# Kernel optimization log

Hardware: AMD Instinct MI355X
Metric: run time of the kernel (lower is better)

## Reference

```python
import jax, jax.numpy as jnp
import numpy as np
import math

D_MODEL = 1024
N_HEAD = 16


def setup_inputs() -> dict:
    key = jax.random.key(0)
    ks = jax.random.split(key, 5)
    x = jax.random.normal(ks[0], (2, 2048, D_MODEL), dtype=jnp.float32)
    # Linear params (torch Linear: y = x @ W.T + b); store as [in, out] for einsum
    s1 = 1.0 / math.sqrt(D_MODEL)
    W_qkv = jax.random.uniform(ks[1], (D_MODEL, 3 * D_MODEL), jnp.float32, -s1, s1)
    b_qkv = jax.random.uniform(ks[2], (3 * D_MODEL,), jnp.float32, -s1, s1)
    W_out = jax.random.uniform(ks[3], (D_MODEL, D_MODEL), jnp.float32, -s1, s1)
    b_out = jax.random.uniform(ks[4], (D_MODEL,), jnp.float32, -s1, s1)
    return {"x": x, "W_qkv": W_qkv, "b_qkv": b_qkv, "W_out": W_out, "b_out": b_out}


def reference(x, W_qkv, b_qkv, W_out, b_out):
    B, L, D = x.shape
    H = N_HEAD
    hd = D // H
    qkv = x @ W_qkv + b_qkv                      # [B, L, 3D]
    q, k, v = jnp.split(qkv, 3, axis=-1)
    # [B, H, L, hd]
    q = q.reshape(B, L, H, hd).transpose(0, 2, 1, 3)
    k = k.reshape(B, L, H, hd).transpose(0, 2, 1, 3)
    v = v.reshape(B, L, H, hd).transpose(0, 2, 1, 3)
    scale = 1.0 / math.sqrt(hd)
    scores = jnp.einsum('bhqd,bhkd->bhqk', q, k) * scale   # [B, H, L, L]
    causal = jnp.tril(jnp.ones((L, L), dtype=bool))
    scores = jnp.where(causal, scores, jnp.float32(-jnp.inf))
    probs = jax.nn.softmax(scores, axis=-1)
    out = jnp.einsum('bhqk,bhkd->bhqd', probs, v)          # [B, H, L, hd]
    out = out.transpose(0, 2, 1, 3).reshape(B, L, D)
    out = out @ W_out + b_out
    return jnp.squeeze(out)
```

## Files before the change

kernel.cpp:

```cpp
#include <hip/hip_runtime.h>
#include <hip/hip_bf16.h>

#define SEQ    2048
#define NHEAD  16
#define HD     64
#define DMODEL 1024

using bf16 = __hip_bfloat16;
using short8 = __attribute__((ext_vector_type(8))) short;
using short4v = __attribute__((ext_vector_type(4))) short;
using f32x4  = __attribute__((ext_vector_type(4))) float;

__device__ __forceinline__ float fast_exp2(float x) {
  return __builtin_amdgcn_exp2f(x);
}
#define WAIT_LGKM0() __builtin_amdgcn_s_waitcnt(0xC07F)

__device__ __forceinline__ void gload_lds16(const bf16* g, bf16* l) {
  __builtin_amdgcn_global_load_lds(
      (const __attribute__((address_space(1))) void*)g,
      (__attribute__((address_space(3))) void*)l, 16, 0, 0);
}


__global__ void prep_k(const float* __restrict__ x, bf16* __restrict__ xb,
                       const float* __restrict__ Wqkv, bf16* __restrict__ WqkvT,
                       const float* __restrict__ Wout, bf16* __restrict__ WoutT) {
  __shared__ bf16 tile[32][33];
  const int id = blockIdx.x, tid = threadIdx.x;
  if (id < 2048) {
    int i = (id * 256 + tid) * 8;
    bf16 tmp[8];
    #pragma unroll
    for (int j = 0; j < 8; ++j) tmp[j] = __float2bfloat16(x[i + j]);
    *(short8*)&xb[i] = *(short8*)tmp;
    return;
  }
  const float* in; bf16* out; int R, C, tx32, ty32;
  if (id < 2048 + 3072) {
    int t = id - 2048; in = Wqkv; out = WqkvT; R = 1024; C = 3072;
    tx32 = t % 96; ty32 = t / 96;
  } else {
    int t = id - 5120; in = Wout; out = WoutT; R = 1024; C = 1024;
    tx32 = t % 32; ty32 = t / 32;
  }
  int c0 = tx32 * 32, r0 = ty32 * 32;
  int tx = tid & 31, ty = tid >> 5;
  #pragma unroll
  for (int i = ty; i < 32; i += 8)
    tile[i][tx] = __float2bfloat16(in[(size_t)(r0 + i) * C + c0 + tx]);
  __syncthreads();
  #pragma unroll
  for (int i = ty; i < 32; i += 8)
    out[(size_t)(c0 + i) * R + r0 + tx] = tile[tx][i];
}

template <int MODE>
__global__ __launch_bounds__(256)
void gemm_bt(const bf16* __restrict__ A, const bf16* __restrict__ BT,
             const float* __restrict__ bias,
             bf16* __restrict__ out0, bf16* __restrict__ out1,
             bf16* __restrict__ out2, float* __restrict__ outf) {
  constexpr int K = 1024;
  __shared__ __align__(16) bf16 As[128 * 32];
  __shared__ __align__(16) bf16 Bs[128 * 32];
  const int tid = threadIdx.x;
  const int wave = tid >> 6, lane = tid & 63;
  const int quad = lane >> 4, l16 = lane & 15;
  const int waveM = (wave >> 1) * 64, waveN = (wave & 1) * 64;
  const int m0 = blockIdx.x * 128, n0 = blockIdx.y * 128;
  const bool swapped = (MODE == 0) && (n0 < 2048);
  const int srow = (lane >> 2);
  const int scol = (((lane & 3) ^ ((lane >> 3) & 3)) * 8);
  const int q8   = (quad ^ ((l16 >> 1) & 3)) * 8;

  const f32x4 zero4 = {0.f, 0.f, 0.f, 0.f};
  f32x4 acc[4][4];
  #pragma unroll
  for (int i = 0; i < 4; ++i)
    #pragma unroll
    for (int j = 0; j < 4; ++j) acc[i][j] = zero4;

  for (int k0 = 0; k0 < K; k0 += 32) {
    __syncthreads();
    #pragma unroll
    for (int half = 0; half < 2; ++half) {
      int grow = half * 64 + wave * 16 + srow;
      gload_lds16(&A [(size_t)(m0 + grow) * K + k0 + scol],
                  &As[(half * 64 + wave * 16) * 32]);
      gload_lds16(&BT[(size_t)(n0 + grow) * K + k0 + scol],
                  &Bs[(half * 64 + wave * 16) * 32]);
    }
    __syncthreads();
    short8 af[4], bfm[4];
    #pragma unroll
    for (int mt = 0; mt < 4; ++mt)
      af[mt] = *(const short8*)&As[(waveM + mt * 16 + l16) * 32 + q8];
    #pragma unroll
    for (int nt = 0; nt < 4; ++nt)
      bfm[nt] = *(const short8*)&Bs[(waveN + nt * 16 + l16) * 32 + q8];
    if (swapped) {
      #pragma unroll
      for (int mt = 0; mt < 4; ++mt)
        #pragma unroll
        for (int nt = 0; nt < 4; ++nt)
          acc[mt][nt] = __builtin_amdgcn_mfma_f32_16x16x32_bf16(
              bfm[nt], af[mt], acc[mt][nt], 0, 0, 0);
    } else {
      #pragma unroll
      for (int mt = 0; mt < 4; ++mt)
        #pragma unroll
        for (int nt = 0; nt < 4; ++nt)
          acc[mt][nt] = __builtin_amdgcn_mfma_f32_16x16x32_bf16(
              af[mt], bfm[nt], acc[mt][nt], 0, 0, 0);
    }
  }

  if (MODE == 1) {
    #pragma unroll
    for (int nt = 0; nt < 4; ++nt) {
      int n = n0 + waveN + nt * 16 + l16;
      float bvv = bias[n];
      #pragma unroll
      for (int mt = 0; mt < 4; ++mt) {
        #pragma unroll
        for (int r = 0; r < 4; ++r) {
          int m = m0 + waveM + mt * 16 + quad * 4 + r;
          outf[(size_t)m * 1024 + n] = acc[mt][nt][r] + bvv;
        }
      }
    }
  } else if (swapped) {
    #pragma unroll
    for (int nt = 0; nt < 4; ++nt) {
      int nb = n0 + waveN + nt * 16 + quad * 4;
      const f32x4 b4 = *(const f32x4*)&bias[nb];
      int oo = nb & 1023;
      int h = oo >> 6, cc = oo & 63;
      bf16* outp = (nb >> 10) ? out1 : out0;
      #pragma unroll
      for (int mt = 0; mt < 4; ++mt) {
        int m = m0 + waveM + mt * 16 + l16;
        int bb = m >> 11, l = m & 2047;
        bf16 tmp[4];
        #pragma unroll
        for (int r = 0; r < 4; ++r)
          tmp[r] = __float2bfloat16(acc[mt][nt][r] + b4[r]);
        *(short4v*)&outp[((size_t)(bb * NHEAD + h) * SEQ + l) * HD + cc] =
            *(short4v*)tmp;
      }
    }
  } else {
    #pragma unroll
    for (int nt = 0; nt < 4; ++nt) {
      int n = n0 + waveN + nt * 16 + l16;
      float bvv = bias[n];
      int oo = n & 1023;
      int h = oo >> 6, cc = oo & 63;
      #pragma unroll
      for (int mt = 0; mt < 4; ++mt) {
        int m = m0 + waveM + mt * 16 + quad * 4;
        int bb = m >> 11, l = m & 2047;
        bf16 tmp[4];
        #pragma unroll
        for (int r = 0; r < 4; ++r)
          tmp[r] = __float2bfloat16(acc[mt][nt][r] + bvv);
        *(short4v*)&out2[((size_t)(bb * NHEAD + h) * HD + cc) * SEQ + l] =
            *(short4v*)tmp;
      }
    }
  }
}

__global__ __launch_bounds__(256, 3)
void attn_k(const bf16* __restrict__ Q, const bf16* __restrict__ Kb,
            const bf16* __restrict__ VT, bf16* __restrict__ O) {
  __shared__ __align__(16) bf16 Ks[2][2][64 * 32];
  __shared__ __align__(16) bf16 Vs[2][2][64 * 32];
  __shared__ __align__(16) bf16 Plds[4][16][72];
  const int tid = threadIdx.x;
  const int wave = tid >> 6, lane = tid & 63;
  const int quad = lane >> 4, l16 = lane & 15;
  const int srow = lane >> 2;
  const int scol = (((lane & 3) ^ ((lane >> 3) & 3)) * 8);
  const int q8   = (quad ^ ((l16 >> 1) & 3)) * 8;
  const int id = blockIdx.x;
  const int bh = id & 31;
  const int qt = 31 - (id >> 5);
  const int b = bh >> 4, h = bh & 15;

  const bf16* Qp = Q  + (size_t)bh * SEQ * HD;
  const bf16* Kp = Kb + (size_t)bh * SEQ * HD;
  const bf16* Vp = VT + (size_t)bh * HD * SEQ;

  const f32x4 zero4 = {0.f, 0.f, 0.f, 0.f};
  const float c = 0.18033688011112042f;
  const float mc = 8.0f * c;

  const int q0w = qt * 64 + wave * 16;
  const int q_lane = q0w + l16;
  const int ntiles = qt + 1;

  short8 qf0 = *(const short8*)&Qp[(size_t)(q0w + l16) * HD + quad * 8];
  short8 qf1 = *(const short8*)&Qp[(size_t)(q0w + l16) * HD + 32 + quad * 8];

  f32x4 oacc[4];
  #pragma unroll
  for (int dt = 0; dt < 4; ++dt) oacc[dt] = zero4;
  float l4[4] = {0.f, 0.f, 0.f, 0.f};

  {
    const int k0 = 0;
    #pragma unroll
    for (int hh = 0; hh < 2; ++hh)
      gload_lds16(&Kp[(size_t)(k0 + wave * 16 + srow) * HD + hh * 32 + scol],
                  &Ks[0][hh][(wave * 16) * 32]);
    #pragma unroll
    for (int ch = 0; ch < 2; ++ch)
      gload_lds16(&Vp[(size_t)(wave * 16 + srow) * SEQ + k0 + ch * 32 + scol],
                  &Vs[0][ch][(wave * 16) * 32]);
  }
  __syncthreads();

  for (int t = 0; t < ntiles; ++t) {
    const int buf = t & 1;
    if (t + 1 < ntiles) {
      const int k1 = (t + 1) << 6, nb = buf ^ 1;
      #pragma unroll
      for (int hh = 0; hh < 2; ++hh)
        gload_lds16(&Kp[(size_t)(k1 + wave * 16 + srow) * HD + hh * 32 + scol],
                    &Ks[nb][hh][(wave * 16) * 32]);
      #pragma unroll
      for (int ch = 0; ch < 2; ++ch)
        gload_lds16(&Vp[(size_t)(wave * 16 + srow) * SEQ + k1 + ch * 32 + scol],
                    &Vs[nb][ch][(wave * 16) * 32]);
    }
    const int k0 = t << 6;

    f32x4 s[4];
    __builtin_amdgcn_s_setprio(1);
    #pragma unroll
    for (int g = 0; g < 4; ++g) {
      short8 ka = *(const short8*)&Ks[buf][0][(g * 16 + l16) * 32 + q8];
      short8 kb = *(const short8*)&Ks[buf][1][(g * 16 + l16) * 32 + q8];
      f32x4 sg = zero4;
      sg = __builtin_amdgcn_mfma_f32_16x16x32_bf16(ka, qf0, sg, 0, 0, 0);
      sg = __builtin_amdgcn_mfma_f32_16x16x32_bf16(kb, qf1, sg, 0, 0, 0);
      s[g] = sg;
    }
    __builtin_amdgcn_s_setprio(0);

    if (t == ntiles - 1) {
      #pragma unroll
      for (int g = 0; g < 4; ++g)
        #pragma unroll
        for (int r = 0; r < 4; ++r) {
          int k = k0 + g * 16 + quad * 4 + r;
          s[g][r] = (k <= q_lane) ? s[g][r] : -__builtin_inff();
        }
    }

    #pragma unroll
    for (int g = 0; g < 4; ++g) {
      bf16 pb[4];
      #pragma unroll
      for (int r = 0; r < 4; ++r) {
        float p = fast_exp2(__builtin_fmaf(s[g][r], c, -mc));
        l4[r] += p;
        pb[r] = __float2bfloat16(p);
      }
      *(short4v*)&Plds[wave][l16][g * 16 + quad * 4] = *(short4v*)pb;
    }
    WAIT_LGKM0();

    __builtin_amdgcn_s_setprio(1);
    #pragma unroll
    for (int ch = 0; ch < 2; ++ch) {
      short8 pf = *(const short8*)&Plds[wave][l16][ch * 32 + quad * 8];
      #pragma unroll
      for (int dt = 0; dt < 4; ++dt) {
        short8 vf = *(const short8*)&Vs[buf][ch][(dt * 16 + l16) * 32 + q8];
        oacc[dt] = __builtin_amdgcn_mfma_f32_16x16x32_bf16(vf, pf, oacc[dt], 0, 0, 0);
      }
    }
    __builtin_amdgcn_s_setprio(0);
    __syncthreads();
  }

  float l_i = (l4[0] + l4[1]) + (l4[2] + l4[3]);
  l_i += __shfl_xor(l_i, 16, 64);
  l_i += __shfl_xor(l_i, 32, 64);
  float inv = 1.f / l_i;

  #pragma unroll
  for (int dt = 0; dt < 4; ++dt) {
    bf16 ob[4];
    #pragma unroll
    for (int r = 0; r < 4; ++r) ob[r] = __float2bfloat16(oacc[dt][r] * inv);
    *(short4v*)&Plds[wave][l16][dt * 16 + quad * 4] = *(short4v*)ob;
  }
  WAIT_LGKM0();
  {
    int row = lane >> 2;
    int col = (lane & 3) * 16;
    short8 o0 = *(const short8*)&Plds[wave][row][col];
    short8 o1 = *(const short8*)&Plds[wave][row][col + 8];
    size_t base = ((size_t)(b * SEQ + q0w + row)) * DMODEL + h * HD + col;
    *(short8*)&O[base]     = o0;
    *(short8*)&O[base + 8] = o1;
  }
}

extern "C" void kernel_launch(void* const* d_in, const int* in_sizes, int n_in,
                              void* d_out, int out_size, void* d_ws, size_t ws_size,
                              hipStream_t stream) {
  const float* x    = (const float*)d_in[0];
  const float* Wqkv = (const float*)d_in[1];
  const float* bqkv = (const float*)d_in[2];
  const float* Wout = (const float*)d_in[3];
  const float* bout = (const float*)d_in[4];
  float* out = (float*)d_out;

  char* ws = (char*)d_ws;
  const size_t MB = 1024 * 1024;
  char* big    = ws + 16384;
  bf16* Kbuf   = (bf16*)(big);
  bf16* VTb    = (bf16*)(big + 8 * MB);
  bf16* xb     = (bf16*)(big + 16 * MB);
  bf16* AO     = (bf16*)(big + 16 * MB);
  bf16* WqkvT  = (bf16*)(big + 24 * MB);
  bf16* WoutT  = (bf16*)(big + 30 * MB);
  bf16* Qb     = (bf16*)d_out;

  prep_k<<<6144, 256, 0, stream>>>(x, xb, Wqkv, WqkvT, Wout, WoutT);
  gemm_bt<0><<<dim3(4096 / 128, 3072 / 128), 256, 0, stream>>>(
      xb, WqkvT, bqkv, Qb, Kbuf, VTb, nullptr);
  attn_k<<<1024, 256, 0, stream>>>(Qb, Kbuf, VTb, AO);
  gemm_bt<1><<<dim3(4096 / 128, 1024 / 128), 256, 0, stream>>>(
      AO, WoutT, bout, nullptr, nullptr, nullptr, out);
}
```

Baseline: 184.4 us.

## Replace QKV GEMM with 256x256-tile, 4-stage pipelined, XCD-aware kernel

Adds a dedicated QKV projection kernel that uses 512 threads and 256x256 output tiles. It streams K-slices through a 4-deep LDS ring buffer using global_load_lds and counted waitcnt, and raises wave priority around the MFMA block. Blocks are mapped so that each XCD gets a contiguous M/N region, which improves L2 reuse. The aim is to cut global traffic per FLOP and hide load latency. In exchange it uses much more LDS and registers, and its 192 blocks leave some imbalance across CUs. The output GEMM is split out into its own non-templated kernel.

```diff
diff --git a/kernel.cpp b/kernel.cpp
--- a/kernel.cpp
+++ b/kernel.cpp
@@ -55,12 +55,140 @@
     out[(size_t)(c0 + i) * R + r0 + tx] = tile[tx][i];
 }
 
-template <int MODE>
+__global__ __launch_bounds__(512, 2)
+void gemm_qkv256(const bf16* __restrict__ A, const bf16* __restrict__ BT,
+                 const float* __restrict__ bias,
+                 bf16* __restrict__ outQ, bf16* __restrict__ outK,
+                 bf16* __restrict__ outV) {
+  constexpr int K = 1024;
+  __shared__ __align__(16) bf16 SA[4][8192];
+  __shared__ __align__(16) bf16 SB[4][8192];
+  const int tid = threadIdx.x;
+  const int wave = tid >> 6, lane = tid & 63;
+  const int quad = lane >> 4, l16 = lane & 15;
+  const int srow = lane >> 2;
+  const int scol = (((lane & 3) ^ ((lane >> 3) & 3)) * 8);
+  const int q8   = (quad ^ ((l16 >> 1) & 3)) * 8;
+  const int waveM = (wave >> 2) * 128, waveN = (wave & 3) * 64;
+
+  const int L = blockIdx.x;
+  const int xcd = L & 7, idx = L >> 3;
+  const int m0 = ((xcd >> 2) * 8 + (idx & 7)) * 256;
+  const int n0 = ((xcd & 3) * 3 + (idx >> 3)) * 256;
+  const bool swapped = n0 < 2048;
+
+  const bf16* aS = A  + (size_t)(m0 + wave * 16 + srow) * K + scol;
+  const bf16* bS = BT + (size_t)(n0 + wave * 16 + srow) * K + scol;
+  bf16* dA = &SA[0][(wave * 16) * 32];
+  bf16* dB = &SB[0][(wave * 16) * 32];
+
+#define STAGE_SLICE(sp)                                                     \
+  {                                                                         \
+    const int rg_ = (sp) & 3, kk_ = (sp) * 32;                              \
+    gload_lds16(aS + kk_,                dA + rg_ * 8192);                  \
+    gload_lds16(aS + 128 * K + kk_,      dA + rg_ * 8192 + 128 * 32);       \
+    gload_lds16(bS + kk_,                dB + rg_ * 8192);                  \
+    gload_lds16(bS + 128 * K + kk_,      dB + rg_ * 8192 + 128 * 32);       \
+  }
+
+  const f32x4 zero4 = {0.f, 0.f, 0.f, 0.f};
+  f32x4 acc[8][4];
+  #pragma unroll
+  for (int i = 0; i < 8; ++i)
+    #pragma unroll
+    for (int j = 0; j < 4; ++j) acc[i][j] = zero4;
+
+  STAGE_SLICE(0);
+  STAGE_SLICE(1);
+  STAGE_SLICE(2);
+
+#define PHASE(s_, WAITN_, DOSTAGE_)                                         \
+  {                                                                         \
+    if (DOSTAGE_) STAGE_SLICE((s_) + 3);                                    \
+    asm volatile("" ::: "memory");                                          \
+    __builtin_amdgcn_s_waitcnt(0xF70 | (WAITN_));   \
+    __builtin_amdgcn_s_barrier();                                           \
+    asm volatile("" ::: "memory");                                          \
+    const bf16* pa = &SA[(s_) & 3][(waveM + l16) * 32 + q8];                \
+    const bf16* pb = &SB[(s_) & 3][(waveN + l16) * 32 + q8];                \
+    short8 af[8], bfr[4];                                                   \
+    _Pragma("unroll")                                                       \
+    for (int mt = 0; mt < 8; ++mt) af[mt] = *(const short8*)(pa + mt * 512);\
+    _Pragma("unroll")                                                       \
+    for (int nt = 0; nt < 4; ++nt) bfr[nt] = *(const short8*)(pb + nt * 512);\
+    __builtin_amdgcn_s_setprio(1);                                          \
+    if (swapped) {                                                          \
+      _Pragma("unroll")                                                     \
+      for (int mt = 0; mt < 8; ++mt)                                        \
+        _Pragma("unroll")                                                   \
+        for (int nt = 0; nt < 4; ++nt)                                      \
+          acc[mt][nt] = __builtin_amdgcn_mfma_f32_16x16x32_bf16(            \
+              bfr[nt], af[mt], acc[mt][nt], 0, 0, 0);                       \
+    } else {                                                                \
+      _Pragma("unroll")                                                     \
+      for (int mt = 0; mt < 8; ++mt)                                        \
+        _Pragma("unroll")                                                   \
+        for (int nt = 0; nt < 4; ++nt)                                      \
+          acc[mt][nt] = __builtin_amdgcn_mfma_f32_16x16x32_bf16(            \
+              af[mt], bfr[nt], acc[mt][nt], 0, 0, 0);                       \
+    }                                                                       \
+    __builtin_amdgcn_s_setprio(0);                                          \
+    asm volatile("" ::: "memory");                                          \
+    __builtin_amdgcn_s_barrier();                                           \
+    asm volatile("" ::: "memory");                                          \
+  }
+
+  #pragma unroll 1
+  for (int s = 0; s < 29; ++s) PHASE(s, 12, true);
+  PHASE(29, 8, false);
+  PHASE(30, 4, false);
+  PHASE(31, 0, false);
+#undef PHASE
+#undef STAGE_SLICE
+
+  if (swapped) {
+    bf16* outp = (n0 >= 1024) ? outK : outQ;
+    #pragma unroll
+    for (int nt = 0; nt < 4; ++nt) {
+      const int nb = n0 + waveN + nt * 16 + quad * 4;
+      const f32x4 b4 = *(const f32x4*)&bias[nb];
+      const int oo = nb & 1023, h = oo >> 6, cc = oo & 63;
+      #pragma unroll
+      for (int mt = 0; mt < 8; ++mt) {
+        const int m = m0 + waveM + mt * 16 + l16;
+        const int bb = m >> 11, l = m & 2047;
+        bf16 tmp[4];
+        #pragma unroll
+        for (int r = 0; r < 4; ++r)
+          tmp[r] = __float2bfloat16(acc[mt][nt][r] + b4[r]);
+        *(short4v*)&outp[((size_t)(bb * NHEAD + h) * SEQ + l) * HD + cc] =
+            *(short4v*)tmp;
+      }
+    }
+  } else {
+    #pragma unroll
+    for (int nt = 0; nt < 4; ++nt) {
+      const int n = n0 + waveN + nt * 16 + l16;
+      const float bv = bias[n];
+      const int oo = n & 1023, h = oo >> 6, cc = oo & 63;
+      #pragma unroll
+      for (int mt = 0; mt < 8; ++mt) {
+        const int m = m0 + waveM + mt * 16 + quad * 4;
+        const int bb = m >> 11, l = m & 2047;
+        bf16 tmp[4];
+        #pragma unroll
+        for (int r = 0; r < 4; ++r)
+          tmp[r] = __float2bfloat16(acc[mt][nt][r] + bv);
+        *(short4v*)&outV[((size_t)(bb * NHEAD + h) * HD + cc) * SEQ + l] =
+            *(short4v*)tmp;
+      }
+    }
+  }
+}
+
 __global__ __launch_bounds__(256)
-void gemm_bt(const bf16* __restrict__ A, const bf16* __restrict__ BT,
-             const float* __restrict__ bias,
-             bf16* __restrict__ out0, bf16* __restrict__ out1,
-             bf16* __restrict__ out2, float* __restrict__ outf) {
+void gemm_out128(const bf16* __restrict__ A, const bf16* __restrict__ BT,
+                 const float* __restrict__ bias, float* __restrict__ outf) {
   constexpr int K = 1024;
   __shared__ __align__(16) bf16 As[128 * 32];
   __shared__ __align__(16) bf16 Bs[128 * 32];
@@ -69,7 +197,6 @@
   const int quad = lane >> 4, l16 = lane & 15;
   const int waveM = (wave >> 1) * 64, waveN = (wave & 1) * 64;
   const int m0 = blockIdx.x * 128, n0 = blockIdx.y * 128;
-  const bool swapped = (MODE == 0) && (n0 < 2048);
   const int srow = (lane >> 2);
   const int scol = (((lane & 3) ^ ((lane >> 3) & 3)) * 8);
   const int q8   = (quad ^ ((l16 >> 1) & 3)) * 8;
@@ -99,74 +226,24 @@
     #pragma unroll
     for (int nt = 0; nt < 4; ++nt)
       bfm[nt] = *(const short8*)&Bs[(waveN + nt * 16 + l16) * 32 + q8];
-    if (swapped) {
-      #pragma unroll
-      for (int mt = 0; mt < 4; ++mt)
-        #pragma unroll
-        for (int nt = 0; nt < 4; ++nt)
-          acc[mt][nt] = __builtin_amdgcn_mfma_f32_16x16x32_bf16(
-              bfm[nt], af[mt], acc[mt][nt], 0, 0, 0);
-    } else {
-      #pragma unroll
-      for (int mt = 0; mt < 4; ++mt)
-        #pragma unroll
-        for (int nt = 0; nt < 4; ++nt)
-          acc[mt][nt] = __builtin_amdgcn_mfma_f32_16x16x32_bf16(
-              af[mt], bfm[nt], acc[mt][nt], 0, 0, 0);
-    }
-  }
-
-  if (MODE == 1) {
-    #pragma unroll
-    for (int nt = 0; nt < 4; ++nt) {
-      int n = n0 + waveN + nt * 16 + l16;
-      float bvv = bias[n];
-      #pragma unroll
-      for (int mt = 0; mt < 4; ++mt) {
-        #pragma unroll
-        for (int r = 0; r < 4; ++r) {
-          int m = m0 + waveM + mt * 16 + quad * 4 + r;
-          outf[(size_t)m * 1024 + n] = acc[mt][nt][r] + bvv;
-        }
-      }
-    }
-  } else if (swapped) {
-    #pragma unroll
-    for (int nt = 0; nt < 4; ++nt) {
-      int nb = n0 + waveN + nt * 16 + quad * 4;
-      const f32x4 b4 = *(const f32x4*)&bias[nb];
-      int oo = nb & 1023;
-      int h = oo >> 6, cc = oo & 63;
-      bf16* outp = (nb >> 10) ? out1 : out0;
-      #pragma unroll
-      for (int mt = 0; mt < 4; ++mt) {
-        int m = m0 + waveM + mt * 16 + l16;
-        int bb = m >> 11, l = m & 2047;
-        bf16 tmp[4];
-        #pragma unroll
-        for (int r = 0; r < 4; ++r)
-          tmp[r] = __float2bfloat16(acc[mt][nt][r] + b4[r]);
-        *(short4v*)&outp[((size_t)(bb * NHEAD + h) * SEQ + l) * HD + cc] =
-            *(short4v*)tmp;
-      }
-    }
-  } else {
-    #pragma unroll
-    for (int nt = 0; nt < 4; ++nt) {
-      int n = n0 + waveN + nt * 16 + l16;
-      float bvv = bias[n];
-      int oo = n & 1023;
-      int h = oo >> 6, cc = oo & 63;
-      #pragma unroll
-      for (int mt = 0; mt < 4; ++mt) {
-        int m = m0 + waveM + mt * 16 + quad * 4;
-        int bb = m >> 11, l = m & 2047;
-        bf16 tmp[4];
-        #pragma unroll
-        for (int r = 0; r < 4; ++r)
-          tmp[r] = __float2bfloat16(acc[mt][nt][r] + bvv);
-        *(short4v*)&out2[((size_t)(bb * NHEAD + h) * HD + cc) * SEQ + l] =
-            *(short4v*)tmp;
+    #pragma unroll
+    for (int mt = 0; mt < 4; ++mt)
+      #pragma unroll
+      for (int nt = 0; nt < 4; ++nt)
+        acc[mt][nt] = __builtin_amdgcn_mfma_f32_16x16x32_bf16(
+            af[mt], bfm[nt], acc[mt][nt], 0, 0, 0);
+  }
+
+  #pragma unroll
+  for (int nt = 0; nt < 4; ++nt) {
+    int n = n0 + waveN + nt * 16 + l16;
+    float bvv = bias[n];
+    #pragma unroll
+    for (int mt = 0; mt < 4; ++mt) {
+      #pragma unroll
+      for (int r = 0; r < 4; ++r) {
+        int m = m0 + waveM + mt * 16 + quad * 4 + r;
+        outf[(size_t)m * 1024 + n] = acc[mt][nt][r] + bvv;
       }
     }
   }
@@ -333,9 +410,8 @@
   bf16* Qb     = (bf16*)d_out;
 
   prep_k<<<6144, 256, 0, stream>>>(x, xb, Wqkv, WqkvT, Wout, WoutT);
-  gemm_bt<0><<<dim3(4096 / 128, 3072 / 128), 256, 0, stream>>>(
-      xb, WqkvT, bqkv, Qb, Kbuf, VTb, nullptr);
+  gemm_qkv256<<<192, 512, 0, stream>>>(xb, WqkvT, bqkv, Qb, Kbuf, VTb);
   attn_k<<<1024, 256, 0, stream>>>(Qb, Kbuf, VTb, AO);
-  gemm_bt<1><<<dim3(4096 / 128, 1024 / 128), 256, 0, stream>>>(
-      AO, WoutT, bout, nullptr, nullptr, nullptr, out);
-}
+  gemm_out128<<<dim3(4096 / 128, 1024 / 128), 256, 0, stream>>>(
+      AO, WoutT, bout, out);
+}
```

Result: slower. 371.2 us (+101.3%).

## Triple-buffer GEMM LDS loads and split QKV projection into two launches

Applied to the files above, without the earlier changes.

Replaces the single-buffered GEMM loop, which synchronized twice per k-step, with a three-stage LDS ring. Loads for step s+2 are issued before computing step s, using explicit vmcnt waits, raw barriers, and raised priority around the MFMAs. The QKV GEMM is split into a Q/K launch and a separate V^T launch, so each kernel has a uniform output layout instead of a per-block branch. The launch bound requests 3 blocks per CU, and LDS use triples, which may limit occupancy. An extra extra launch is added, and a stray dead load expression is left in the epilogue.

```diff
diff --git a/kernel.cpp b/kernel.cpp
--- a/kernel.cpp
+++ b/kernel.cpp
@@ -56,23 +56,38 @@
 }
 
 template <int MODE>
-__global__ __launch_bounds__(256)
-void gemm_bt(const bf16* __restrict__ A, const bf16* __restrict__ BT,
-             const float* __restrict__ bias,
-             bf16* __restrict__ out0, bf16* __restrict__ out1,
-             bf16* __restrict__ out2, float* __restrict__ outf) {
+__global__ __launch_bounds__(256, 3)
+void gemm_p(const bf16* __restrict__ A, const bf16* __restrict__ BT,
+            const float* __restrict__ bias,
+            bf16* __restrict__ o0, bf16* __restrict__ o1,
+            float* __restrict__ outf) {
   constexpr int K = 1024;
-  __shared__ __align__(16) bf16 As[128 * 32];
-  __shared__ __align__(16) bf16 Bs[128 * 32];
+  constexpr int NS = K / 32;
+  __shared__ __align__(16) bf16 SA[3][4096];
+  __shared__ __align__(16) bf16 SB[3][4096];
   const int tid = threadIdx.x;
   const int wave = tid >> 6, lane = tid & 63;
   const int quad = lane >> 4, l16 = lane & 15;
-  const int waveM = (wave >> 1) * 64, waveN = (wave & 1) * 64;
-  const int m0 = blockIdx.x * 128, n0 = blockIdx.y * 128;
-  const bool swapped = (MODE == 0) && (n0 < 2048);
-  const int srow = (lane >> 2);
+  const int srow = lane >> 2;
   const int scol = (((lane & 3) ^ ((lane >> 3) & 3)) * 8);
   const int q8   = (quad ^ ((l16 >> 1) & 3)) * 8;
+  const int waveM = (wave >> 1) * 64, waveN = (wave & 1) * 64;
+  const int m0 = blockIdx.x * 128;
+  const int n0 = (MODE == 2 ? 2048 : 0) + blockIdx.y * 128;
+
+  const bf16* aS = A  + (size_t)(m0 + wave * 16 + srow) * K + scol;
+  const bf16* bS = BT + (size_t)(n0 + wave * 16 + srow) * K + scol;
+  bf16* dA = &SA[0][(wave * 16) * 32];
+  bf16* dB = &SB[0][(wave * 16) * 32];
+
+#define STAGE(sp_, rg_)                                                    \
+  {                                                                        \
+    const int kk_ = (sp_) * 32;                                            \
+    gload_lds16(aS + kk_,           dA + (rg_) * 4096);                    \
+    gload_lds16(aS + 64 * K + kk_,  dA + (rg_) * 4096 + 64 * 32);          \
+    gload_lds16(bS + kk_,           dB + (rg_) * 4096);                    \
+    gload_lds16(bS + 64 * K + kk_,  dB + (rg_) * 4096 + 64 * 32);          \
+  }
 
   const f32x4 zero4 = {0.f, 0.f, 0.f, 0.f};
   f32x4 acc[4][4];
@@ -81,40 +96,53 @@
     #pragma unroll
     for (int j = 0; j < 4; ++j) acc[i][j] = zero4;
 
-  for (int k0 = 0; k0 < K; k0 += 32) {
-    __syncthreads();
-    #pragma unroll
-    for (int half = 0; half < 2; ++half) {
-      int grow = half * 64 + wave * 16 + srow;
-      gload_lds16(&A [(size_t)(m0 + grow) * K + k0 + scol],
-                  &As[(half * 64 + wave * 16) * 32]);
-      gload_lds16(&BT[(size_t)(n0 + grow) * K + k0 + scol],
-                  &Bs[(half * 64 + wave * 16) * 32]);
-    }
-    __syncthreads();
-    short8 af[4], bfm[4];
-    #pragma unroll
-    for (int mt = 0; mt < 4; ++mt)
-      af[mt] = *(const short8*)&As[(waveM + mt * 16 + l16) * 32 + q8];
-    #pragma unroll
-    for (int nt = 0; nt < 4; ++nt)
-      bfm[nt] = *(const short8*)&Bs[(waveN + nt * 16 + l16) * 32 + q8];
-    if (swapped) {
-      #pragma unroll
-      for (int mt = 0; mt < 4; ++mt)
-        #pragma unroll
-        for (int nt = 0; nt < 4; ++nt)
-          acc[mt][nt] = __builtin_amdgcn_mfma_f32_16x16x32_bf16(
-              bfm[nt], af[mt], acc[mt][nt], 0, 0, 0);
-    } else {
-      #pragma unroll
-      for (int mt = 0; mt < 4; ++mt)
-        #pragma unroll
-        for (int nt = 0; nt < 4; ++nt)
-          acc[mt][nt] = __builtin_amdgcn_mfma_f32_16x16x32_bf16(
-              af[mt], bfm[nt], acc[mt][nt], 0, 0, 0);
-    }
-  }
+  STAGE(0, 0);
+  STAGE(1, 1);
+
+#define PHASE(s_, rg_, WAITN_, DOSTAGE_, srg_)                             \
+  {                                                                        \
+    if (DOSTAGE_) STAGE((s_) + 2, (srg_));                                 \
+    asm volatile("" ::: "memory");                                         \
+    __builtin_amdgcn_s_waitcnt(0xF70 | (WAITN_));       \
+    __builtin_amdgcn_s_barrier();                                          \
+    asm volatile("" ::: "memory");                                         \
+    const bf16* pa = &SA[(rg_)][(waveM + l16) * 32 + q8];                  \
+    const bf16* pb = &SB[(rg_)][(waveN + l16) * 32 + q8];                  \
+    short8 af[4], bfm[4];                                                  \
+    _Pragma("unroll")                                                      \
+    for (int mt = 0; mt < 4; ++mt) af[mt] = *(const short8*)(pa + mt * 512);\
+    _Pragma("unroll")                                                      \
+    for (int nt = 0; nt < 4; ++nt) bfm[nt] = *(const short8*)(pb + nt * 512);\
+    __builtin_amdgcn_s_setprio(1);                                         \
+    _Pragma("unroll")                                                      \
+    for (int mt = 0; mt < 4; ++mt)                                         \
+      _Pragma("unroll")                                                    \
+      for (int nt = 0; nt < 4; ++nt)                                       \
+        acc[mt][nt] = (MODE == 0)                                          \
+          ? __builtin_amdgcn_mfma_f32_16x16x32_bf16(                       \
+                bfm[nt], af[mt], acc[mt][nt], 0, 0, 0)                     \
+          : __builtin_amdgcn_mfma_f32_16x16x32_bf16(                       \
+                af[mt], bfm[nt], acc[mt][nt], 0, 0, 0);                    \
+    __builtin_amdgcn_s_setprio(0);                                         \
+    asm volatile("" ::: "memory");                                         \
+    __builtin_amdgcn_s_barrier();                                          \
+    asm volatile("" ::: "memory");                                         \
+  }
+
+  {
+    int rg = 0, srg = 2;
+    #pragma unroll 1
+    for (int s = 0; s < NS - 2; ++s) {
+      PHASE(s, rg, 8, true, srg);
+      rg  = (rg  == 2) ? 0 : rg + 1;
+      srg = (srg == 2) ? 0 : srg + 1;
+    }
+    PHASE(NS - 2, rg, 4, false, 0);
+    rg = (rg == 2) ? 0 : rg + 1;
+    PHASE(NS - 1, rg, 0, false, 0);
+  }
+#undef PHASE
+#undef STAGE
 
   if (MODE == 1) {
     #pragma unroll
@@ -130,22 +158,22 @@
         }
       }
     }
-  } else if (swapped) {
+  } else if (MODE == 0) {
     #pragma unroll
     for (int nt = 0; nt < 4; ++nt) {
-      int nb = n0 + waveN + nt * 16 + quad * 4;
+      const int nb = n0 + waveN + nt * 16 + quad * 4;
       const f32x4 b4 = *(const f32x4*)&bias[nb];
-      int oo = nb & 1023;
-      int h = oo >> 6, cc = oo & 63;
-      bf16* outp = (nb >> 10) ? out1 : out0;
+      const int oo = nb & 1023, h = oo >> 6, cc = oo & 63;
+      bf16* outp = (nb >= 1024) ? o1 : o0;
       #pragma unroll
       for (int mt = 0; mt < 4; ++mt) {
-        int m = m0 + waveM + mt * 16 + l16;
-        int bb = m >> 11, l = m & 2047;
+        const int m = m0 + waveM + mt * 16 + l16;
+        const int bb = m >> 11, l = m & 2047;
         bf16 tmp[4];
         #pragma unroll
         for (int r = 0; r < 4; ++r)
           tmp[r] = __float2bfloat16(acc[mt][nt][r] + b4[r]);
+        *(short4v*)&o0[0];
         *(short4v*)&outp[((size_t)(bb * NHEAD + h) * SEQ + l) * HD + cc] =
             *(short4v*)tmp;
       }
@@ -153,19 +181,18 @@
   } else {
     #pragma unroll
     for (int nt = 0; nt < 4; ++nt) {
-      int n = n0 + waveN + nt * 16 + l16;
-      float bvv = bias[n];
-      int oo = n & 1023;
-      int h = oo >> 6, cc = oo & 63;
+      const int n = n0 + waveN + nt * 16 + l16;
+      const float bv = bias[n];
+      const int oo = n & 1023, h = oo >> 6, cc = oo & 63;
       #pragma unroll
       for (int mt = 0; mt < 4; ++mt) {
-        int m = m0 + waveM + mt * 16 + quad * 4;
-        int bb = m >> 11, l = m & 2047;
+        const int m = m0 + waveM + mt * 16 + quad * 4;
+        const int bb = m >> 11, l = m & 2047;
         bf16 tmp[4];
         #pragma unroll
         for (int r = 0; r < 4; ++r)
-          tmp[r] = __float2bfloat16(acc[mt][nt][r] + bvv);
-        *(short4v*)&out2[((size_t)(bb * NHEAD + h) * HD + cc) * SEQ + l] =
+          tmp[r] = __float2bfloat16(acc[mt][nt][r] + bv);
+        *(short4v*)&o0[((size_t)(bb * NHEAD + h) * HD + cc) * SEQ + l] =
             *(short4v*)tmp;
       }
     }
@@ -333,9 +360,11 @@
   bf16* Qb     = (bf16*)d_out;
 
   prep_k<<<6144, 256, 0, stream>>>(x, xb, Wqkv, WqkvT, Wout, WoutT);
-  gemm_bt<0><<<dim3(4096 / 128, 3072 / 128), 256, 0, stream>>>(
-      xb, WqkvT, bqkv, Qb, Kbuf, VTb, nullptr);
+  gemm_p<0><<<dim3(32, 16), 256, 0, stream>>>(
+      xb, WqkvT, bqkv, Qb, Kbuf, nullptr);
+  gemm_p<2><<<dim3(32, 8), 256, 0, stream>>>(
+      xb, WqkvT, bqkv, VTb, nullptr, nullptr);
   attn_k<<<1024, 256, 0, stream>>>(Qb, Kbuf, VTb, AO);
-  gemm_bt<1><<<dim3(4096 / 128, 1024 / 128), 256, 0, stream>>>(
-      AO, WoutT, bout, nullptr, nullptr, nullptr, out);
-}
+  gemm_p<1><<<dim3(32, 8), 256, 0, stream>>>(
+      AO, WoutT, bout, nullptr, nullptr, out);
+}
```

New measurement: 190.0 us. +3.0%, slower.
